# Kernel tuning notes

Measured on AMD Instinct MI355X. Metric: run time of the kernel, lower is better.

## Reference

```python
import jax, jax.numpy as jnp
import numpy as np

IGNORE_LABEL = 255
THRESH = 0.7
MIN_KEPT = 262144


def setup_inputs() -> dict:
    key = jax.random.key(0)
    k1, k2 = jax.random.split(key)
    pred = jax.random.normal(k1, (8, 19, 768, 768), dtype=jnp.float32)
    target = jax.random.randint(k2, (8, 768, 768), 0, 19, dtype=jnp.int32)
    return {"pred": pred, "target": target}


def reference(pred, target):
    b, c, h, w = pred.shape
    n = b * h * w

    t = target.reshape(-1)                      # [N]
    valid = t != IGNORE_LABEL                   # [N] bool
    tc = jnp.where(valid, t, 0)                 # clamp ignored labels to 0 for gather
    num_valid = valid.sum()

    # pred.transpose(0,1).reshape(c,-1) in torch flattens (b,h,w) b-major,
    # matching target.view(-1); here we use [N, C] layout instead.
    logits = jnp.transpose(pred, (0, 2, 3, 1)).reshape(n, c)  # [N, C]
    logp = jax.nn.log_softmax(logits, axis=-1)                # [N, C]
    logp_t = jnp.take_along_axis(logp, tc[:, None], axis=-1)[:, 0]  # [N]

    # prob of the ground-truth class; invalid pixels masked to 1 (never "hard")
    mask_prob = jnp.where(valid, jnp.exp(logp_t), 1.0)        # [N]

    # k-th smallest gt-prob defines the OHEM threshold (raised if > thresh)
    k = min(n, MIN_KEPT)
    kth = jnp.sort(mask_prob)[k - 1]
    threshold = jnp.maximum(kth, THRESH)
    kept = mask_prob <= threshold

    # torch: OHEM applies only when min_kept <= num_valid and num_valid > 0
    do_ohem = (num_valid > 0) & (num_valid >= MIN_KEPT)
    valid_f = jnp.where(do_ohem, valid & kept, valid)

    # CrossEntropyLoss(reduction='mean', ignore_index=ignore_label)
    pix_loss = -logp_t                                        # [N]
    denom = jnp.maximum(valid_f.sum(), 1).astype(pred.dtype)
    loss = jnp.sum(jnp.where(valid_f, pix_loss, 0.0)) / denom
    return loss
```

## Files before the change

kernel.cpp:

```cpp
#include <hip/hip_runtime.h>


#define CC 19
#define HWSZ 589824
#define NPIX 4718592
#define KSEL 262144
#define IGNORE_LBL 255
#define THR 0.7f
#define NBLK 1152
#define ITERS 4

#define HIST1_OFF 8
#define HIST2_OFF (HIST1_OFF + 2048)
#define HIST3_OFF (HIST2_OFF + 2048)
#define META_WORDS 8192
#define PROB_OFF META_WORDS

__global__ __launch_bounds__(256) void k_init(unsigned* __restrict__ ws) {
    for (int i = threadIdx.x; i < META_WORDS; i += 256) ws[i] = 0u;
}

template <int NBINS>
__device__ __forceinline__ void find_bin(const unsigned* __restrict__ gh,
                                         unsigned krem_in, int shift,
                                         unsigned& sel_io, unsigned& krem_out) {
    constexpr int CHUNK = NBINS / 256;
    __shared__ unsigned csum[256];
    __shared__ unsigned sb[2];
    const int t = threadIdx.x;
    __syncthreads();
    unsigned loc[CHUNK];
    unsigned s = 0;
#pragma unroll
    for (int j = 0; j < CHUNK; ++j) { loc[j] = gh[t * CHUNK + j]; s += loc[j]; }
    csum[t] = s;
    for (int off = 1; off < 256; off <<= 1) {
        __syncthreads();
        unsigned add = (t >= off) ? csum[t - off] : 0u;
        __syncthreads();
        csum[t] += add;
    }
    unsigned incl = csum[t];
    unsigned excl = incl - s;
    if (excl < krem_in && krem_in <= incl) {
        unsigned run = excl;
        unsigned bin = 0;
        bool found = false;
#pragma unroll
        for (int j = 0; j < CHUNK; ++j) {
            unsigned nrun = run + loc[j];
            if (!found && nrun >= krem_in) { bin = (unsigned)(t * CHUNK + j); found = true; }
            if (!found) run = nrun;
        }
        sb[0] = bin;
        sb[1] = krem_in - run;
    }
    __syncthreads();
    sel_io |= sb[0] << shift;
    krem_out = sb[1];
}

__global__ __launch_bounds__(256) void k_pass1(const float* __restrict__ pred,
                                               const int* __restrict__ target,
                                               unsigned* __restrict__ ws) {
    __shared__ unsigned hist[2048];
    for (int i = threadIdx.x; i < 2048; i += 256) hist[i] = 0u;
    __syncthreads();

    unsigned nv = 0;
    for (int it = 0; it < ITERS; ++it) {
        int q = it * (NBLK * 256) + blockIdx.x * 256 + threadIdx.x;
        int pix0 = q * 4;
        int b = pix0 / HWSZ;
        int hw = pix0 - b * HWSZ;
        const float* base = pred + (size_t)b * ((size_t)CC * HWSZ) + hw;

        float x[CC][4];
#pragma unroll
        for (int c = 0; c < CC; ++c) {
            float4 v = *reinterpret_cast<const float4*>(base + (size_t)c * HWSZ);
            x[c][0] = v.x; x[c][1] = v.y; x[c][2] = v.z; x[c][3] = v.w;
        }
        int4 t4 = *reinterpret_cast<const int4*>(target + pix0);
        int tt[4] = {t4.x, t4.y, t4.z, t4.w};

        unsigned pb[4];
#pragma unroll
        for (int p = 0; p < 4; ++p) {
            int t = tt[p];
            bool valid = (t != IGNORE_LBL);
            nv += valid ? 1u : 0u;
            int tc = valid ? t : 0;
            float m = x[0][p];
#pragma unroll
            for (int c = 1; c < CC; ++c) m = fmaxf(m, x[c][p]);
            float s = 0.0f;
            float xt = x[0][p];
#pragma unroll
            for (int c = 0; c < CC; ++c) {
                float v = x[c][p];
                s += expf(v - m);
                xt = (c == tc) ? v : xt;
            }
            float lp = xt - m - logf(s);
            float pr = valid ? expf(lp) : 1.0f;
            pb[p] = __float_as_uint(pr);
            atomicAdd(&hist[pb[p] >> 21], 1u);
        }
        *reinterpret_cast<uint4*>(ws + PROB_OFF + pix0) =
            make_uint4(pb[0], pb[1], pb[2], pb[3]);
    }

    for (int off = 32; off; off >>= 1) nv += __shfl_down(nv, off);
    if ((threadIdx.x & 63) == 0) atomicAdd(ws + 0, nv);

    __syncthreads();
    int rot = (blockIdx.x & 7) << 8;
    for (int i = threadIdx.x; i < 2048; i += 256) {
        int idx = (i + rot) & 2047;
        unsigned v = hist[idx];
        if (v) atomicAdd(ws + HIST1_OFF + idx, v);
    }
}

template <int LEVEL>
__global__ __launch_bounds__(256) void k_refine(unsigned* __restrict__ ws) {
    constexpr int NB = (LEVEL == 2) ? 2048 : 1024;
    __shared__ unsigned hist[NB];
    for (int i = threadIdx.x; i < NB; i += 256) hist[i] = 0u;
    unsigned sel = 0, krem = 0;
    find_bin<2048>(ws + HIST1_OFF, (unsigned)KSEL, 21, sel, krem);
    if (LEVEL == 3) find_bin<2048>(ws + HIST2_OFF, krem, 10, sel, krem);

    const uint4* pbv = reinterpret_cast<const uint4*>(ws + PROB_OFF);
    for (int it = 0; it < ITERS; ++it) {
        int q = it * (NBLK * 256) + blockIdx.x * 256 + threadIdx.x;
        uint4 v = pbv[q];
        unsigned a[4] = {v.x, v.y, v.z, v.w};
#pragma unroll
        for (int p = 0; p < 4; ++p) {
            unsigned bits = a[p];
            if (LEVEL == 2) {
                if ((bits >> 21) == (sel >> 21))
                    atomicAdd(&hist[(bits >> 10) & 2047u], 1u);
            } else {
                if ((bits >> 10) == (sel >> 10))
                    atomicAdd(&hist[bits & 1023u], 1u);
            }
        }
    }
    __syncthreads();
    unsigned* gh = ws + ((LEVEL == 2) ? HIST2_OFF : HIST3_OFF);
    int rot = (blockIdx.x & 3) << 8;
    for (int i = threadIdx.x; i < NB; i += 256) {
        int idx = (i + rot) & (NB - 1);
        unsigned v = hist[idx];
        if (v) atomicAdd(gh + idx, v);
    }
}

__global__ __launch_bounds__(256) void k_final(unsigned* __restrict__ ws,
                                               const int* __restrict__ target) {
    unsigned sel = 0, krem = 0;
    find_bin<2048>(ws + HIST1_OFF, (unsigned)KSEL, 21, sel, krem);
    find_bin<2048>(ws + HIST2_OFF, krem, 10, sel, krem);
    find_bin<1024>(ws + HIST3_OFF, krem, 0, sel, krem);
    float thr = fmaxf(__uint_as_float(sel), THR);
    unsigned nvv = ws[0];
    bool do_ohem = (nvv > 0u) && (nvv >= (unsigned)KSEL);

    const uint4* pbv = reinterpret_cast<const uint4*>(ws + PROB_OFF);
    float ls = 0.0f;
    unsigned lc = 0;
    for (int it = 0; it < ITERS; ++it) {
        int q = it * (NBLK * 256) + blockIdx.x * 256 + threadIdx.x;
        int pix0 = q * 4;
        uint4 v = pbv[q];
        int4 t4 = *reinterpret_cast<const int4*>(target + pix0);
        unsigned a[4] = {v.x, v.y, v.z, v.w};
        int tt[4] = {t4.x, t4.y, t4.z, t4.w};
#pragma unroll
        for (int p = 0; p < 4; ++p) {
            bool valid = (tt[p] != IGNORE_LBL);
            float pr = __uint_as_float(a[p]);
            bool kept = (pr <= thr);
            bool vf = do_ohem ? (valid && kept) : valid;
            if (vf) { ls += -logf(pr); lc += 1u; }
        }
    }
    for (int off = 32; off; off >>= 1) {
        ls += __shfl_down(ls, off);
        lc += __shfl_down(lc, off);
    }
    __shared__ float wsum[4];
    __shared__ unsigned wcnt[4];
    if ((threadIdx.x & 63) == 0) {
        wsum[threadIdx.x >> 6] = ls;
        wcnt[threadIdx.x >> 6] = lc;
    }
    __syncthreads();
    if (threadIdx.x == 0) {
        float bs = wsum[0] + wsum[1] + wsum[2] + wsum[3];
        unsigned bc = wcnt[0] + wcnt[1] + wcnt[2] + wcnt[3];
        atomicAdd(reinterpret_cast<double*>(ws + 6), (double)bs);
        atomicAdd(ws + 3, bc);
    }
}

__global__ void k_finalize(const unsigned* __restrict__ ws, float* __restrict__ out) {
    if (threadIdx.x == 0 && blockIdx.x == 0) {
        double s = *reinterpret_cast<const double*>(ws + 6);
        unsigned c = ws[3];
        unsigned d = (c > 0u) ? c : 1u;
        out[0] = (float)(s / (double)d);
    }
}

extern "C" void kernel_launch(void* const* d_in, const int* in_sizes, int n_in,
                              void* d_out, int out_size, void* d_ws, size_t ws_size,
                              hipStream_t stream) {
    const float* pred = (const float*)d_in[0];
    const int* target = (const int*)d_in[1];
    unsigned* ws = (unsigned*)d_ws;
    float* out = (float*)d_out;

    k_init<<<1, 256, 0, stream>>>(ws);
    k_pass1<<<NBLK, 256, 0, stream>>>(pred, target, ws);
    k_refine<2><<<NBLK, 256, 0, stream>>>(ws);
    k_refine<3><<<NBLK, 256, 0, stream>>>(ws);
    k_final<<<NBLK, 256, 0, stream>>>(ws, target);
    k_finalize<<<1, 64, 0, stream>>>(ws, out);
}
```

Measured before the change: 579.7 us.

## Speculatively accumulate loss at fixed threshold and skip refine passes when valid

Pass1 now also accumulates the cross-entropy sum and count for all valid pixels and for pixels with prob <= 0.7. If the coarse histogram shows at least KSEL pixels below the 0.7 bin, the k-th value cannot exceed the threshold, so the refine and final kernels exit early and finalize uses the speculative sums. This is meant to skip two histogram refinement passes and the final loss pass over the stored probability buffer. In exchange pass1 carries more registers and atomics, and the early check depends on the bin boundary matching 0.7.

```diff
diff --git a/kernel.cpp b/kernel.cpp
--- a/kernel.cpp
+++ b/kernel.cpp
@@ -9,8 +9,16 @@
 #define THR 0.7f
 #define NBLK 1152
 #define ITERS 4
-
-#define HIST1_OFF 8
+#define BIN_07 505
+
+#define W_SPEC_CNT 1
+#define W_TOT_CNT 2
+#define W_SLOW_CNT 3
+#define W_EARLY 4
+#define W_SLOW_SUM 6
+#define W_SPEC_SUM 8
+#define W_TOT_SUM 10
+#define HIST1_OFF 16
 #define HIST2_OFF (HIST1_OFF + 2048)
 #define HIST3_OFF (HIST2_OFF + 2048)
 #define META_WORDS 8192
@@ -18,6 +26,18 @@
 
 __global__ __launch_bounds__(256) void k_init(unsigned* __restrict__ ws) {
     for (int i = threadIdx.x; i < META_WORDS; i += 256) ws[i] = 0u;
+}
+
+__device__ __forceinline__ bool early_thr(const unsigned* __restrict__ gh) {
+    unsigned v = 0;
+    for (int i = threadIdx.x; i < BIN_07; i += 256) v += gh[i];
+    for (int off = 32; off; off >>= 1) v += __shfl_down(v, off);
+    __shared__ unsigned cw[4];
+    if ((threadIdx.x & 63) == 0) cw[threadIdx.x >> 6] = v;
+    __syncthreads();
+    unsigned c_lo = cw[0] + cw[1] + cw[2] + cw[3];
+    __syncthreads();
+    return c_lo >= (unsigned)KSEL;
 }
 
 template <int NBINS>
@@ -67,7 +87,9 @@
     for (int i = threadIdx.x; i < 2048; i += 256) hist[i] = 0u;
     __syncthreads();
 
-    unsigned nv = 0;
+    float ls_spec = 0.0f, ls_tot = 0.0f;
+    unsigned lc_spec = 0, lc_tot = 0;
+
     for (int it = 0; it < ITERS; ++it) {
         int q = it * (NBLK * 256) + blockIdx.x * 256 + threadIdx.x;
         int pix0 = q * 4;
@@ -89,7 +111,6 @@
         for (int p = 0; p < 4; ++p) {
             int t = tt[p];
             bool valid = (t != IGNORE_LBL);
-            nv += valid ? 1u : 0u;
             int tc = valid ? t : 0;
             float m = x[0][p];
 #pragma unroll
@@ -106,15 +127,37 @@
             float pr = valid ? expf(lp) : 1.0f;
             pb[p] = __float_as_uint(pr);
             atomicAdd(&hist[pb[p] >> 21], 1u);
+            if (valid) {
+                ls_tot += -lp; lc_tot += 1u;
+                if (pr <= THR) { ls_spec += -lp; lc_spec += 1u; }
+            }
         }
         *reinterpret_cast<uint4*>(ws + PROB_OFF + pix0) =
             make_uint4(pb[0], pb[1], pb[2], pb[3]);
     }
 
-    for (int off = 32; off; off >>= 1) nv += __shfl_down(nv, off);
-    if ((threadIdx.x & 63) == 0) atomicAdd(ws + 0, nv);
-
-    __syncthreads();
+    for (int off = 32; off; off >>= 1) {
+        ls_spec += __shfl_down(ls_spec, off);
+        ls_tot  += __shfl_down(ls_tot, off);
+        lc_spec += __shfl_down(lc_spec, off);
+        lc_tot  += __shfl_down(lc_tot, off);
+    }
+    __shared__ float fs[2][4];
+    __shared__ unsigned us[2][4];
+    if ((threadIdx.x & 63) == 0) {
+        int w = threadIdx.x >> 6;
+        fs[0][w] = ls_spec; fs[1][w] = ls_tot;
+        us[0][w] = lc_spec; us[1][w] = lc_tot;
+    }
+    __syncthreads();
+    if (threadIdx.x == 0) {
+        atomicAdd(reinterpret_cast<double*>(ws + W_SPEC_SUM),
+                  (double)(fs[0][0] + fs[0][1] + fs[0][2] + fs[0][3]));
+        atomicAdd(reinterpret_cast<double*>(ws + W_TOT_SUM),
+                  (double)(fs[1][0] + fs[1][1] + fs[1][2] + fs[1][3]));
+        atomicAdd(ws + W_SPEC_CNT, us[0][0] + us[0][1] + us[0][2] + us[0][3]);
+        atomicAdd(ws + W_TOT_CNT, us[1][0] + us[1][1] + us[1][2] + us[1][3]);
+    }
     int rot = (blockIdx.x & 7) << 8;
     for (int i = threadIdx.x; i < 2048; i += 256) {
         int idx = (i + rot) & 2047;
@@ -125,6 +168,8 @@
 
 template <int LEVEL>
 __global__ __launch_bounds__(256) void k_refine(unsigned* __restrict__ ws) {
+    if (early_thr(ws + HIST1_OFF)) return;
+
     constexpr int NB = (LEVEL == 2) ? 2048 : 1024;
     __shared__ unsigned hist[NB];
     for (int i = threadIdx.x; i < NB; i += 256) hist[i] = 0u;
@@ -161,13 +206,17 @@
 
 __global__ __launch_bounds__(256) void k_final(unsigned* __restrict__ ws,
                                                const int* __restrict__ target) {
+    bool early = early_thr(ws + HIST1_OFF);
+    unsigned tot_cnt = ws[W_TOT_CNT];
+    bool do_ohem = (tot_cnt > 0u) && (tot_cnt >= (unsigned)KSEL);
+    if (blockIdx.x == 0 && threadIdx.x == 0) ws[W_EARLY] = early ? 1u : 0u;
+    if (early || !do_ohem) return;
+
     unsigned sel = 0, krem = 0;
     find_bin<2048>(ws + HIST1_OFF, (unsigned)KSEL, 21, sel, krem);
     find_bin<2048>(ws + HIST2_OFF, krem, 10, sel, krem);
     find_bin<1024>(ws + HIST3_OFF, krem, 0, sel, krem);
     float thr = fmaxf(__uint_as_float(sel), THR);
-    unsigned nvv = ws[0];
-    bool do_ohem = (nvv > 0u) && (nvv >= (unsigned)KSEL);
 
     const uint4* pbv = reinterpret_cast<const uint4*>(ws + PROB_OFF);
     float ls = 0.0f;
@@ -183,9 +232,8 @@
         for (int p = 0; p < 4; ++p) {
             bool valid = (tt[p] != IGNORE_LBL);
             float pr = __uint_as_float(a[p]);
-            bool kept = (pr <= thr);
-            bool vf = do_ohem ? (valid && kept) : valid;
-            if (vf) { ls += -logf(pr); lc += 1u; }
+            bool vf = valid && (pr <= thr);
+            if (vf) { ls += -logf(fmaxf(pr, 1e-37f)); lc += 1u; }
         }
     }
     for (int off = 32; off; off >>= 1) {
@@ -200,17 +248,25 @@
     }
     __syncthreads();
     if (threadIdx.x == 0) {
-        float bs = wsum[0] + wsum[1] + wsum[2] + wsum[3];
-        unsigned bc = wcnt[0] + wcnt[1] + wcnt[2] + wcnt[3];
-        atomicAdd(reinterpret_cast<double*>(ws + 6), (double)bs);
-        atomicAdd(ws + 3, bc);
+        atomicAdd(reinterpret_cast<double*>(ws + W_SLOW_SUM),
+                  (double)(wsum[0] + wsum[1] + wsum[2] + wsum[3]));
+        atomicAdd(ws + W_SLOW_CNT, wcnt[0] + wcnt[1] + wcnt[2] + wcnt[3]);
     }
 }
 
 __global__ void k_finalize(const unsigned* __restrict__ ws, float* __restrict__ out) {
     if (threadIdx.x == 0 && blockIdx.x == 0) {
-        double s = *reinterpret_cast<const double*>(ws + 6);
-        unsigned c = ws[3];
+        unsigned tot_cnt = ws[W_TOT_CNT];
+        bool do_ohem = (tot_cnt > 0u) && (tot_cnt >= (unsigned)KSEL);
+        double s;
+        unsigned c;
+        if (!do_ohem) {
+            s = *reinterpret_cast<const double*>(ws + W_TOT_SUM);  c = tot_cnt;
+        } else if (ws[W_EARLY]) {
+            s = *reinterpret_cast<const double*>(ws + W_SPEC_SUM); c = ws[W_SPEC_CNT];
+        } else {
+            s = *reinterpret_cast<const double*>(ws + W_SLOW_SUM); c = ws[W_SLOW_CNT];
+        }
         unsigned d = (c > 0u) ? c : 1u;
         out[0] = (float)(s / (double)d);
     }
```

New measurement: 511.7 us. 1.13x faster.
